# Kernel tuning notes

Measured on AMD Instinct MI355X. Metric: run time of the kernel, lower is better.

## Reference

```python
import jax, jax.numpy as jnp
import numpy as np

N_NODES = 50000
N_EDGES = 800000
IN_FEAT = 128
HEADS = 8
HEAD_DIM = 16  # out_feat // num_heads = 128 // 8
NEG_SLOPE = 0.2


def setup_inputs() -> dict:
    key = jax.random.key(0)
    ks = jax.random.split(key, 8)
    g = 1.0 / np.sqrt(IN_FEAT)
    return {
        "x": jax.random.normal(ks[0], (N_NODES, IN_FEAT), jnp.float32),
        "efeat": jax.random.normal(ks[1], (N_EDGES, IN_FEAT), jnp.float32),
        "src": jax.random.randint(ks[2], (N_EDGES,), 0, N_NODES),
        "dst": jax.random.randint(ks[3], (N_EDGES,), 0, N_NODES),
        "W_src": jax.random.normal(ks[4], (HEADS * HEAD_DIM, IN_FEAT), jnp.float32) * g,
        "b_src": jnp.zeros((HEADS * HEAD_DIM,), jnp.float32),
        "W_dst": jax.random.normal(ks[5], (HEADS * HEAD_DIM, IN_FEAT), jnp.float32) * g,
        "b_dst": jnp.zeros((HEADS * HEAD_DIM,), jnp.float32),
        "W_edge": jax.random.normal(ks[6], (HEADS * HEAD_DIM, IN_FEAT), jnp.float32) * g,
        "attn": jax.random.normal(ks[7], (HEADS, HEAD_DIM), jnp.float32) * (1.0 / np.sqrt(HEAD_DIM)),
    }


def reference(x, efeat, src, dst, W_src, b_src, W_dst, b_dst, W_edge, attn):
    H, D = HEADS, HEAD_DIM
    # node/edge projections: [N,H,D] / [E,H,D]
    feat_src = (x @ W_src.T + b_src).reshape(-1, H, D)
    feat_dst = (x @ W_dst.T + b_dst).reshape(-1, H, D)
    feat_edge = (efeat @ W_edge.T).reshape(-1, H, D)

    # per-edge GATv2 score: LeakyReLU(src + dst + edge) . attn  -> [E,H]
    fs = feat_src[src]                                    # gather [E,H,D]
    tmp = fs + feat_dst[dst] + feat_edge
    e = jnp.where(tmp >= 0, tmp, NEG_SLOPE * tmp)
    score = jnp.einsum('ehd,hd->eh', e, attn)

    # edge softmax normalized per destination node
    m = jax.ops.segment_max(score, dst, num_segments=N_NODES)     # [N,H]
    ex = jnp.exp(score - jax.lax.stop_gradient(m)[dst])
    z = jax.ops.segment_sum(ex, dst, num_segments=N_NODES)        # [N,H]
    a = ex / z[dst]                                               # [E,H]

    # weighted scatter-sum of (src + edge) messages
    msg = (fs + feat_edge) * a[:, :, None]                        # [E,H,D]
    h = jax.ops.segment_sum(msg, dst, num_segments=N_NODES)       # [N,H,D]

    # res_fc is None since in_feat == H*D; activation = relu
    h = jax.nn.relu(h)
    return h.reshape(N_NODES, H * D)
```

## Files before the change

### kernel.cpp

```cpp
#include <hip/hip_runtime.h>
#include <hip/hip_bf16.h>

#define NNODES 50000
#define NEDGES 800000
#define NEG_SLOPE 0.2f
#define N_PAD 50176

typedef float f32x4 __attribute__((ext_vector_type(4)));
typedef float f32x2 __attribute__((ext_vector_type(2)));
typedef __bf16 bf16x8 __attribute__((ext_vector_type(8)));
typedef __bf16 bf16x4 __attribute__((ext_vector_type(4)));
typedef __bf16 bf16x2 __attribute__((ext_vector_type(2)));

__global__ __launch_bounds__(256) void convert_hist(
    const float* __restrict__ W0, const float* __restrict__ W1,
    const float* __restrict__ W2, __bf16* __restrict__ out,
    const int* __restrict__ dst, int* __restrict__ deg, int* __restrict__ arr)
{
  int b = blockIdx.x;
  if (b < 48) {
    int m = b >> 4;
    const float* W = (m == 0) ? W0 : ((m == 1) ? W1 : W2);
    __bf16* o = out + m * 16384;
    int i = (b & 15) * 1024 + threadIdx.x * 4;
    int r = i >> 7, cx = i & 127;
    f32x4 v = *(const f32x4*)(W + i);
    int kb = cx >> 3, ko = cx & 7;
    int off = r * 128 + ((kb ^ (r & 15)) << 3) + ko;
    bf16x4 pk = { (__bf16)v.x, (__bf16)v.y, (__bf16)v.z, (__bf16)v.w };
    *(bf16x4*)(o + off) = pk;
  } else {
    int e = (b - 48) * 256 + threadIdx.x;
    arr[e] = atomicAdd(&deg[dst[e]], 1);
  }
}

__global__ void scan_local(const int* __restrict__ deg, int* __restrict__ scanned,
                           int* __restrict__ bsum){
  __shared__ int s[1024];
  int t = threadIdx.x, i = blockIdx.x * 1024 + t;
  int v = deg[i];
  s[t] = v; __syncthreads();
  #pragma unroll
  for (int off = 1; off < 1024; off <<= 1){
    int x = (t >= off) ? s[t - off] : 0;
    __syncthreads();
    s[t] += x;
    __syncthreads();
  }
  scanned[i] = s[t] - v;
  if (t == 1023) bsum[blockIdx.x] = s[t];
}

__global__ void scan_add(const int* __restrict__ scanned, const int* __restrict__ bsum,
                         int* __restrict__ row_start){
  __shared__ int sbase;
  int b = blockIdx.x, t = threadIdx.x;
  if (t == 0){
    int lim = b >> 2, acc = 0;
    for (int j = 0; j < lim; ++j) acc += bsum[j];
    sbase = acc;
  }
  __syncthreads();
  int i = b * 256 + t;
  if (i < N_PAD) row_start[i] = scanned[i] + sbase;
}

__device__ __forceinline__ void gemm_core(
    int m0, const float* __restrict__ A, const __bf16* __restrict__ Wsw,
    int M, __bf16* sS, f32x4 (&acc)[2][8])
{
  const int t = threadIdx.x;
  #pragma unroll
  for (int it = 0; it < 8; ++it) {
    int lin = it * 2048 + t * 8;
    *(bf16x8*)(sS + lin) = *(const bf16x8*)(Wsw + lin);
  }

  const int w = t >> 6, lane = t & 63;
  const int rsel = lane & 15, quad = lane >> 4;

  bf16x8 af[4][2];
  #pragma unroll
  for (int mi = 0; mi < 2; ++mi) {
    int gr = m0 + w * 32 + mi * 16 + rsel;
    const float* p = A + (size_t)gr * 128 + (quad << 3);
    bool ok = gr < M;
    f32x4 r0[4], r1[4];
    #pragma unroll
    for (int kk = 0; kk < 4; ++kk) {
      f32x4 z4 = {0.f, 0.f, 0.f, 0.f};
      r0[kk] = ok ? *(const f32x4*)(p + kk * 32)     : z4;
      r1[kk] = ok ? *(const f32x4*)(p + kk * 32 + 4) : z4;
    }
    #pragma unroll
    for (int kk = 0; kk < 4; ++kk)
      af[kk][mi] = (bf16x8){ (__bf16)r0[kk].x, (__bf16)r0[kk].y, (__bf16)r0[kk].z, (__bf16)r0[kk].w,
                             (__bf16)r1[kk].x, (__bf16)r1[kk].y, (__bf16)r1[kk].z, (__bf16)r1[kk].w };
  }

  f32x4 zero = {0.f, 0.f, 0.f, 0.f};
  #pragma unroll
  for (int mi = 0; mi < 2; ++mi)
    #pragma unroll
    for (int ni = 0; ni < 8; ++ni) acc[mi][ni] = zero;

  __syncthreads();

  #pragma unroll
  for (int kk = 0; kk < 4; ++kk) {
    int kb0 = kk * 4 + quad;
    bf16x8 bfr[8];
    #pragma unroll
    for (int ni = 0; ni < 8; ++ni) {
      int r = ni * 16 + rsel;
      bfr[ni] = *(const bf16x8*)(sS + r * 128 + ((kb0 ^ (r & 15)) << 3));
    }
    #pragma unroll
    for (int mi = 0; mi < 2; ++mi)
      #pragma unroll
      for (int ni = 0; ni < 8; ++ni)
        acc[mi][ni] = __builtin_amdgcn_mfma_f32_16x16x32_bf16(af[kk][mi], bfr[ni], acc[mi][ni], 0, 0, 0);
  }
}

__global__ __launch_bounds__(256, 4) void proj_all(
    const float* __restrict__ x, const float* __restrict__ efeat,
    const __bf16* __restrict__ wsw, const float* __restrict__ b_src,
    const float* __restrict__ b_dst,
    const int* __restrict__ src, const int* __restrict__ dst,
    const int* __restrict__ arr, const int* __restrict__ row_start,
    float* __restrict__ feat_src, float* __restrict__ feat_dst,
    __bf16* __restrict__ fe, int* __restrict__ src_perm)
{
  __shared__ __bf16 sS[128 * 136];
  int b = blockIdx.x;
  const int t = threadIdx.x;
  f32x4 acc[2][8];

  if (b < 6250) {
    int m0 = b * 128;
    gemm_core(m0, efeat, wsw + 32768, NEDGES, sS, acc);

    const int w = t >> 6, lane = t & 63;
    const int rsel = lane & 15, quad = lane >> 4;

    __syncthreads();
    #pragma unroll
    for (int mi = 0; mi < 2; ++mi)
      #pragma unroll
      for (int ni = 0; ni < 8; ++ni)
        #pragma unroll
        for (int r4 = 0; r4 < 4; ++r4) {
          float v = acc[mi][ni][r4];
          float vx = __shfl_xor(v, 1);
          if (!(rsel & 1)) {
            int trow = w * 32 + mi * 16 + quad * 4 + r4;
            bf16x2 pkv = { (__bf16)v, (__bf16)vx };
            *(bf16x2*)(sS + trow * 136 + ni * 16 + rsel) = pkv;
          }
        }
    __syncthreads();
    int tr = t >> 1, h = t & 1;
    int e = m0 + tr;
    int pos = row_start[dst[e]] + arr[e];
    if (h == 0) src_perm[pos] = src[e];
    const __bf16* sp = sS + tr * 136 + h * 64;
    __bf16* dp = fe + (size_t)pos * 128 + h * 64;
    #pragma unroll
    for (int i = 0; i < 8; ++i)
      *(bf16x8*)(dp + i * 8) = *(const bf16x8*)(sp + i * 8);
  } else {
    const float* bias;
    float* outp;
    int m0;
    if (b < 6641) { m0 = (b - 6250) * 128; bias = b_src; outp = feat_src; }
    else          { m0 = (b - 6641) * 128; bias = b_dst; outp = feat_dst; }
    gemm_core(m0, x, b < 6641 ? wsw : wsw + 16384, NNODES, sS, acc);

    const int w = t >> 6, lane = t & 63;
    const int rsel = lane & 15, quad = lane >> 4;
    #pragma unroll
    for (int mi = 0; mi < 2; ++mi)
      #pragma unroll
      for (int ni = 0; ni < 8; ++ni)
        #pragma unroll
        for (int r4 = 0; r4 < 4; ++r4) {
          int grow = m0 + w * 32 + mi * 16 + quad * 4 + r4;
          int col = ni * 16 + rsel;
          if (grow < NNODES)
            outp[(size_t)grow * 128 + col] = acc[mi][ni][r4] + bias[col];
        }
  }
}

__global__ __launch_bounds__(256) void aggregate_fused(
    const int* __restrict__ row_start, const int* __restrict__ deg,
    const int* __restrict__ src_perm, const float* __restrict__ fs,
    const float* __restrict__ fd, const __bf16* __restrict__ fe,
    const float* __restrict__ attn, float* __restrict__ out)
{
  int wv = threadIdx.x >> 6, lane = threadIdx.x & 63;
  int n = blockIdx.x * 4 + wv;
  int row = row_start[n], dg = deg[n];
  int c = lane << 1;
  f32x2 fdv = *(const f32x2*)(fd + (size_t)n * 128 + c);
  f32x2 atv = *(const f32x2*)(attn + c);
  float acc0 = 0.f, acc1 = 0.f, zs = 0.f;
  const __bf16* fep = fe + (size_t)row * 128 + c;

  #define EDGE_BODY(FV, EV)                                            \
    {                                                                  \
      float v0 = (FV).x + (float)(EV).x;                               \
      float v1 = (FV).y + (float)(EV).y;                               \
      float t0 = v0 + fdv.x; t0 = t0 >= 0.f ? t0 : NEG_SLOPE * t0;     \
      float t1 = v1 + fdv.y; t1 = t1 >= 0.f ? t1 : NEG_SLOPE * t1;     \
      float p = t0 * atv.x + t1 * atv.y;                               \
      p += __shfl_xor(p, 1);                                           \
      p += __shfl_xor(p, 2);                                           \
      p += __shfl_xor(p, 4);                                           \
      float ex = __expf(p);                                            \
      acc0 += ex * v0; acc1 += ex * v1; zs += ex;                      \
    }

  for (int base = 0; base < dg; base += 64){
    int cnt = min(64, dg - base);
    int si = 0;
    if (lane < cnt) si = src_perm[row + base + lane];
    int j = 0;
    for (; j + 8 <= cnt; j += 8){
      int sx[8];
      f32x2 fx[8];
      bf16x2 ex[8];
      #pragma unroll
      for (int u = 0; u < 8; ++u) sx[u] = __shfl(si, j + u, 64);
      #pragma unroll
      for (int u = 0; u < 8; ++u) fx[u] = *(const f32x2*)(fs + (size_t)sx[u] * 128 + c);
      #pragma unroll
      for (int u = 0; u < 8; ++u) ex[u] = *(const bf16x2*)(fep + (size_t)(base + j + u) * 128);
      #pragma unroll
      for (int u = 0; u < 8; ++u) EDGE_BODY(fx[u], ex[u])
    }
    for (; j < cnt; ++j){
      int s0 = __shfl(si, j, 64);
      f32x2 f0 = *(const f32x2*)(fs + (size_t)s0 * 128 + c);
      bf16x2 e0 = *(const bf16x2*)(fep + (size_t)(base + j) * 128);
      EDGE_BODY(f0, e0)
    }
  }
  #undef EDGE_BODY

  float rz = zs > 0.f ? 1.f / zs : 0.f;
  float o0 = acc0 * rz, o1 = acc1 * rz;
  f32x2 ov = { o0 > 0.f ? o0 : 0.f, o1 > 0.f ? o1 : 0.f };
  *(f32x2*)(out + (size_t)n * 128 + c) = ov;
}

extern "C" void kernel_launch(void* const* d_in, const int* in_sizes, int n_in,
                              void* d_out, int out_size, void* d_ws, size_t ws_size,
                              hipStream_t stream)
{
  const float* x      = (const float*)d_in[0];
  const float* efeat  = (const float*)d_in[1];
  const int*   src    = (const int*)d_in[2];
  const int*   dst    = (const int*)d_in[3];
  const float* W_src  = (const float*)d_in[4];
  const float* b_src  = (const float*)d_in[5];
  const float* W_dst  = (const float*)d_in[6];
  const float* b_dst  = (const float*)d_in[7];
  const float* W_edge = (const float*)d_in[8];
  const float* attn   = (const float*)d_in[9];

  char* ws = (char*)d_ws;
  float*  feat_src  = (float*)(ws + 0);
  float*  feat_dst  = (float*)(ws + 25600000);
  __bf16* fe        = (__bf16*)(ws + 51200000);
  int*    src_perm  = (int*)  (ws + 256000000);
  int*    arr       = (int*)  (ws + 259200000);
  int*    row_start = (int*)  (ws + 262400000);
  int*    scanned   = (int*)  (ws + 262601408);
  int*    deg       = (int*)  (ws + 262802112);
  int*    bsum      = (int*)  (ws + 263002816);
  __bf16* wsw       = (__bf16*)(ws + 263003840);

  hipMemsetAsync(deg, 0, 200704, stream);

  convert_hist<<<3173, 256, 0, stream>>>(W_src, W_dst, W_edge, wsw, dst, deg, arr);

  scan_local<<<49, 1024, 0, stream>>>(deg, scanned, bsum);
  scan_add  <<<196, 256, 0, stream>>>(scanned, bsum, row_start);

  proj_all<<<7032, 256, 0, stream>>>(x, efeat, wsw, b_src, b_dst,
                                     src, dst, arr, row_start,
                                     feat_src, feat_dst, fe, src_perm);

  aggregate_fused<<<12500, 256, 0, stream>>>(row_start, deg, src_perm, feat_src,
                                             feat_dst, fe, attn, (float*)d_out);
}
```

Before: 815.0 us.

## Precompute src+edge messages in edge projection, drop gather from aggregation

The node projections now run before the edge projection, fused into the same launch as the scan-add step. The edge projection kernel gathers feat_src for each edge and writes the bf16 sum (src+edge) directly in dst-sorted order. The aggregation kernel then streams contiguous messages with no src_perm lookup and no random feat_src gathers. This moves the random gather into a kernel that reads full contiguous 512-byte rows. In exchange, the src feature is rounded to bf16 before the score and accumulation, and one launch's worth of overlap is lost. The weight-to-LDS load is also reordered so global loads are issued before the LDS stores.

```diff
diff --git a/kernel.cpp b/kernel.cpp
--- a/kernel.cpp
+++ b/kernel.cpp
@@ -52,52 +52,46 @@
   if (t == 1023) bsum[blockIdx.x] = s[t];
 }
 
-__global__ void scan_add(const int* __restrict__ scanned, const int* __restrict__ bsum,
-                         int* __restrict__ row_start){
-  __shared__ int sbase;
-  int b = blockIdx.x, t = threadIdx.x;
-  if (t == 0){
-    int lim = b >> 2, acc = 0;
-    for (int j = 0; j < lim; ++j) acc += bsum[j];
-    sbase = acc;
-  }
-  __syncthreads();
-  int i = b * 256 + t;
-  if (i < N_PAD) row_start[i] = scanned[i] + sbase;
-}
-
 __device__ __forceinline__ void gemm_core(
     int m0, const float* __restrict__ A, const __bf16* __restrict__ Wsw,
     int M, __bf16* sS, f32x4 (&acc)[2][8])
 {
   const int t = threadIdx.x;
-  #pragma unroll
-  for (int it = 0; it < 8; ++it) {
-    int lin = it * 2048 + t * 8;
-    *(bf16x8*)(sS + lin) = *(const bf16x8*)(Wsw + lin);
-  }
-
   const int w = t >> 6, lane = t & 63;
   const int rsel = lane & 15, quad = lane >> 4;
 
-  bf16x8 af[4][2];
+  bf16x8 wreg[8];
+  #pragma unroll
+  for (int it = 0; it < 8; ++it)
+    wreg[it] = *(const bf16x8*)(Wsw + it * 2048 + t * 8);
+
+  f32x4 r0[2][4], r1[2][4];
   #pragma unroll
   for (int mi = 0; mi < 2; ++mi) {
     int gr = m0 + w * 32 + mi * 16 + rsel;
     const float* p = A + (size_t)gr * 128 + (quad << 3);
     bool ok = gr < M;
-    f32x4 r0[4], r1[4];
     #pragma unroll
     for (int kk = 0; kk < 4; ++kk) {
       f32x4 z4 = {0.f, 0.f, 0.f, 0.f};
-      r0[kk] = ok ? *(const f32x4*)(p + kk * 32)     : z4;
-      r1[kk] = ok ? *(const f32x4*)(p + kk * 32 + 4) : z4;
-    }
+      r0[mi][kk] = ok ? *(const f32x4*)(p + kk * 32)     : z4;
+      r1[mi][kk] = ok ? *(const f32x4*)(p + kk * 32 + 4) : z4;
+    }
+  }
+
+  #pragma unroll
+  for (int it = 0; it < 8; ++it)
+    *(bf16x8*)(sS + it * 2048 + t * 8) = wreg[it];
+
+  bf16x8 af[4][2];
+  #pragma unroll
+  for (int mi = 0; mi < 2; ++mi)
     #pragma unroll
     for (int kk = 0; kk < 4; ++kk)
-      af[kk][mi] = (bf16x8){ (__bf16)r0[kk].x, (__bf16)r0[kk].y, (__bf16)r0[kk].z, (__bf16)r0[kk].w,
-                             (__bf16)r1[kk].x, (__bf16)r1[kk].y, (__bf16)r1[kk].z, (__bf16)r1[kk].w };
-  }
+      af[kk][mi] = (bf16x8){ (__bf16)r0[mi][kk].x, (__bf16)r0[mi][kk].y,
+                             (__bf16)r0[mi][kk].z, (__bf16)r0[mi][kk].w,
+                             (__bf16)r1[mi][kk].x, (__bf16)r1[mi][kk].y,
+                             (__bf16)r1[mi][kk].z, (__bf16)r1[mi][kk].w };
 
   f32x4 zero = {0.f, 0.f, 0.f, 0.f};
   #pragma unroll
@@ -124,80 +118,113 @@
   }
 }
 
-__global__ __launch_bounds__(256, 4) void proj_all(
-    const float* __restrict__ x, const float* __restrict__ efeat,
-    const __bf16* __restrict__ wsw, const float* __restrict__ b_src,
-    const float* __restrict__ b_dst,
+__global__ __launch_bounds__(256, 4) void scan_nodes(
+    const int* __restrict__ scanned, const int* __restrict__ bsum,
+    int* __restrict__ row_start,
+    const float* __restrict__ x, const __bf16* __restrict__ wsw,
+    const float* __restrict__ b_src, const float* __restrict__ b_dst,
+    float* __restrict__ feat_src, float* __restrict__ feat_dst)
+{
+  __shared__ __bf16 sS[128 * 136];
+  __shared__ int sbase;
+  int b = blockIdx.x;
+  if (b < 196) {
+    int t = threadIdx.x;
+    if (t == 0){
+      int lim = b >> 2, a = 0;
+      for (int j = 0; j < lim; ++j) a += bsum[j];
+      sbase = a;
+    }
+    __syncthreads();
+    int i = b * 256 + t;
+    if (i < N_PAD) row_start[i] = scanned[i] + sbase;
+    return;
+  }
+  const float* bias; float* outp; int m0; const __bf16* wp;
+  if (b < 587) { m0 = (b - 196) * 128; bias = b_src; outp = feat_src; wp = wsw; }
+  else         { m0 = (b - 587) * 128; bias = b_dst; outp = feat_dst; wp = wsw + 16384; }
+
+  f32x4 acc[2][8];
+  gemm_core(m0, x, wp, NNODES, sS, acc);
+
+  const int t = threadIdx.x;
+  const int w = t >> 6, lane = t & 63;
+  const int rsel = lane & 15, quad = lane >> 4;
+  #pragma unroll
+  for (int mi = 0; mi < 2; ++mi)
+    #pragma unroll
+    for (int ni = 0; ni < 8; ++ni)
+      #pragma unroll
+      for (int r4 = 0; r4 < 4; ++r4) {
+        int grow = m0 + w * 32 + mi * 16 + quad * 4 + r4;
+        int col = ni * 16 + rsel;
+        if (grow < NNODES)
+          outp[(size_t)grow * 128 + col] = acc[mi][ni][r4] + bias[col];
+      }
+}
+
+__global__ __launch_bounds__(256, 4) void proj_edge(
+    const float* __restrict__ efeat, const __bf16* __restrict__ Wsw,
     const int* __restrict__ src, const int* __restrict__ dst,
     const int* __restrict__ arr, const int* __restrict__ row_start,
-    float* __restrict__ feat_src, float* __restrict__ feat_dst,
-    __bf16* __restrict__ fe, int* __restrict__ src_perm)
+    const float* __restrict__ fs, __bf16* __restrict__ msg)
 {
   __shared__ __bf16 sS[128 * 136];
-  int b = blockIdx.x;
   const int t = threadIdx.x;
+  const int m0 = blockIdx.x * 128;
+
+  int tr = t >> 1, h = t & 1;
+  int e = m0 + tr;
+  int s = src[e];
+  int pos = row_start[dst[e]] + arr[e];
+
   f32x4 acc[2][8];
-
-  if (b < 6250) {
-    int m0 = b * 128;
-    gemm_core(m0, efeat, wsw + 32768, NEDGES, sS, acc);
-
-    const int w = t >> 6, lane = t & 63;
-    const int rsel = lane & 15, quad = lane >> 4;
-
-    __syncthreads();
-    #pragma unroll
-    for (int mi = 0; mi < 2; ++mi)
+  gemm_core(m0, efeat, Wsw, NEDGES, sS, acc);
+
+  const int w = t >> 6, lane = t & 63;
+  const int rsel = lane & 15, quad = lane >> 4;
+
+  __syncthreads();
+  #pragma unroll
+  for (int mi = 0; mi < 2; ++mi)
+    #pragma unroll
+    for (int ni = 0; ni < 8; ++ni)
       #pragma unroll
-      for (int ni = 0; ni < 8; ++ni)
-        #pragma unroll
-        for (int r4 = 0; r4 < 4; ++r4) {
-          float v = acc[mi][ni][r4];
-          float vx = __shfl_xor(v, 1);
-          if (!(rsel & 1)) {
-            int trow = w * 32 + mi * 16 + quad * 4 + r4;
-            bf16x2 pkv = { (__bf16)v, (__bf16)vx };
-            *(bf16x2*)(sS + trow * 136 + ni * 16 + rsel) = pkv;
-          }
+      for (int r4 = 0; r4 < 4; ++r4) {
+        float v = acc[mi][ni][r4];
+        float vx = __shfl_xor(v, 1);
+        if (!(rsel & 1)) {
+          int trow = w * 32 + mi * 16 + quad * 4 + r4;
+          bf16x2 pkv = { (__bf16)v, (__bf16)vx };
+          *(bf16x2*)(sS + trow * 136 + ni * 16 + rsel) = pkv;
         }
-    __syncthreads();
-    int tr = t >> 1, h = t & 1;
-    int e = m0 + tr;
-    int pos = row_start[dst[e]] + arr[e];
-    if (h == 0) src_perm[pos] = src[e];
-    const __bf16* sp = sS + tr * 136 + h * 64;
-    __bf16* dp = fe + (size_t)pos * 128 + h * 64;
+      }
+  __syncthreads();
+
+  const float* fsp = fs + (size_t)s * 128 + h * 64;
+  const __bf16* sp = sS + tr * 136 + h * 64;
+  __bf16* dp = msg + (size_t)pos * 128 + h * 64;
+  #pragma unroll
+  for (int half = 0; half < 2; ++half) {
+    f32x4 fr[8];
     #pragma unroll
     for (int i = 0; i < 8; ++i)
-      *(bf16x8*)(dp + i * 8) = *(const bf16x8*)(sp + i * 8);
-  } else {
-    const float* bias;
-    float* outp;
-    int m0;
-    if (b < 6641) { m0 = (b - 6250) * 128; bias = b_src; outp = feat_src; }
-    else          { m0 = (b - 6641) * 128; bias = b_dst; outp = feat_dst; }
-    gemm_core(m0, x, b < 6641 ? wsw : wsw + 16384, NNODES, sS, acc);
-
-    const int w = t >> 6, lane = t & 63;
-    const int rsel = lane & 15, quad = lane >> 4;
-    #pragma unroll
-    for (int mi = 0; mi < 2; ++mi)
+      fr[i] = *(const f32x4*)(fsp + half * 32 + i * 4);
+    #pragma unroll
+    for (int i = 0; i < 4; ++i) {
+      bf16x8 ev = *(const bf16x8*)(sp + half * 32 + i * 8);
+      bf16x8 mv;
       #pragma unroll
-      for (int ni = 0; ni < 8; ++ni)
-        #pragma unroll
-        for (int r4 = 0; r4 < 4; ++r4) {
-          int grow = m0 + w * 32 + mi * 16 + quad * 4 + r4;
-          int col = ni * 16 + rsel;
-          if (grow < NNODES)
-            outp[(size_t)grow * 128 + col] = acc[mi][ni][r4] + bias[col];
-        }
-  }
-}
-
-__global__ __launch_bounds__(256) void aggregate_fused(
+      for (int j = 0; j < 8; ++j)
+        mv[j] = (__bf16)(fr[i * 2 + (j >> 2)][j & 3] + (float)ev[j]);
+      *(bf16x8*)(dp + half * 32 + i * 8) = mv;
+    }
+  }
+}
+
+__global__ __launch_bounds__(256) void aggregate_msg(
     const int* __restrict__ row_start, const int* __restrict__ deg,
-    const int* __restrict__ src_perm, const float* __restrict__ fs,
-    const float* __restrict__ fd, const __bf16* __restrict__ fe,
+    const __bf16* __restrict__ msg, const float* __restrict__ fd,
     const float* __restrict__ attn, float* __restrict__ out)
 {
   int wv = threadIdx.x >> 6, lane = threadIdx.x & 63;
@@ -206,13 +233,12 @@
   int c = lane << 1;
   f32x2 fdv = *(const f32x2*)(fd + (size_t)n * 128 + c);
   f32x2 atv = *(const f32x2*)(attn + c);
-  float acc0 = 0.f, acc1 = 0.f, zs = 0.f;
-  const __bf16* fep = fe + (size_t)row * 128 + c;
-
-  #define EDGE_BODY(FV, EV)                                            \
+  float a0 = 0.f, a1 = 0.f, zs = 0.f;
+  const __bf16* mp = msg + (size_t)row * 128 + c;
+
+  #define EDGE_BODY(MV)                                                \
     {                                                                  \
-      float v0 = (FV).x + (float)(EV).x;                               \
-      float v1 = (FV).y + (float)(EV).y;                               \
+      float v0 = (float)(MV).x, v1 = (float)(MV).y;                    \
       float t0 = v0 + fdv.x; t0 = t0 >= 0.f ? t0 : NEG_SLOPE * t0;     \
       float t1 = v1 + fdv.y; t1 = t1 >= 0.f ? t1 : NEG_SLOPE * t1;     \
       float p = t0 * atv.x + t1 * atv.y;                               \
@@ -220,38 +246,25 @@
       p += __shfl_xor(p, 2);                                           \
       p += __shfl_xor(p, 4);                                           \
       float ex = __expf(p);                                            \
-      acc0 += ex * v0; acc1 += ex * v1; zs += ex;                      \
-    }
-
-  for (int base = 0; base < dg; base += 64){
-    int cnt = min(64, dg - base);
-    int si = 0;
-    if (lane < cnt) si = src_perm[row + base + lane];
-    int j = 0;
-    for (; j + 8 <= cnt; j += 8){
-      int sx[8];
-      f32x2 fx[8];
-      bf16x2 ex[8];
-      #pragma unroll
-      for (int u = 0; u < 8; ++u) sx[u] = __shfl(si, j + u, 64);
-      #pragma unroll
-      for (int u = 0; u < 8; ++u) fx[u] = *(const f32x2*)(fs + (size_t)sx[u] * 128 + c);
-      #pragma unroll
-      for (int u = 0; u < 8; ++u) ex[u] = *(const bf16x2*)(fep + (size_t)(base + j + u) * 128);
-      #pragma unroll
-      for (int u = 0; u < 8; ++u) EDGE_BODY(fx[u], ex[u])
-    }
-    for (; j < cnt; ++j){
-      int s0 = __shfl(si, j, 64);
-      f32x2 f0 = *(const f32x2*)(fs + (size_t)s0 * 128 + c);
-      bf16x2 e0 = *(const bf16x2*)(fep + (size_t)(base + j) * 128);
-      EDGE_BODY(f0, e0)
-    }
+      a0 += ex * v0; a1 += ex * v1; zs += ex;                          \
+    }
+
+  int j = 0;
+  for (; j + 8 <= dg; j += 8) {
+    bf16x2 mv[8];
+    #pragma unroll
+    for (int u = 0; u < 8; ++u) mv[u] = *(const bf16x2*)(mp + (size_t)(j + u) * 128);
+    #pragma unroll
+    for (int u = 0; u < 8; ++u) EDGE_BODY(mv[u])
+  }
+  for (; j < dg; ++j) {
+    bf16x2 mv = *(const bf16x2*)(mp + (size_t)j * 128);
+    EDGE_BODY(mv)
   }
   #undef EDGE_BODY
 
   float rz = zs > 0.f ? 1.f / zs : 0.f;
-  float o0 = acc0 * rz, o1 = acc1 * rz;
+  float o0 = a0 * rz, o1 = a1 * rz;
   f32x2 ov = { o0 > 0.f ? o0 : 0.f, o1 > 0.f ? o1 : 0.f };
   *(f32x2*)(out + (size_t)n * 128 + c) = ov;
 }
@@ -274,26 +287,26 @@
   char* ws = (char*)d_ws;
   float*  feat_src  = (float*)(ws + 0);
   float*  feat_dst  = (float*)(ws + 25600000);
-  __bf16* fe        = (__bf16*)(ws + 51200000);
-  int*    src_perm  = (int*)  (ws + 256000000);
-  int*    arr       = (int*)  (ws + 259200000);
-  int*    row_start = (int*)  (ws + 262400000);
-  int*    scanned   = (int*)  (ws + 262601408);
-  int*    deg       = (int*)  (ws + 262802112);
-  int*    bsum      = (int*)  (ws + 263002816);
-  __bf16* wsw       = (__bf16*)(ws + 263003840);
+  __bf16* msg       = (__bf16*)(ws + 51200000);
+  int*    arr       = (int*)  (ws + 256000000);
+  int*    row_start = (int*)  (ws + 259200000);
+  int*    scanned   = (int*)  (ws + 259400704);
+  int*    deg       = (int*)  (ws + 259601408);
+  int*    bsum      = (int*)  (ws + 259802112);
+  __bf16* wsw       = (__bf16*)(ws + 259803136);
 
   hipMemsetAsync(deg, 0, 200704, stream);
 
   convert_hist<<<3173, 256, 0, stream>>>(W_src, W_dst, W_edge, wsw, dst, deg, arr);
 
   scan_local<<<49, 1024, 0, stream>>>(deg, scanned, bsum);
-  scan_add  <<<196, 256, 0, stream>>>(scanned, bsum, row_start);
-
-  proj_all<<<7032, 256, 0, stream>>>(x, efeat, wsw, b_src, b_dst,
-                                     src, dst, arr, row_start,
-                                     feat_src, feat_dst, fe, src_perm);
-
-  aggregate_fused<<<12500, 256, 0, stream>>>(row_start, deg, src_perm, feat_src,
-                                             feat_dst, fe, attn, (float*)d_out);
-}
+
+  scan_nodes<<<978, 256, 0, stream>>>(scanned, bsum, row_start, x, wsw,
+                                      b_src, b_dst, feat_src, feat_dst);
+
+  proj_edge<<<6250, 256, 0, stream>>>(efeat, wsw + 32768, src, dst, arr, row_start,
+                                      feat_src, msg);
+
+  aggregate_msg<<<12500, 256, 0, stream>>>(row_start, deg, msg, feat_dst, attn,
+                                           (float*)d_out);
+}
```

Result: faster. 782.1 us (-4.0%).
